# Optimization experiments

Hardware: AMD Instinct MI355X
Metric: run time of the kernel (lower is better)

Reference implementation:

```python
import jax, jax.numpy as jnp
import numpy as np

B, POMO, PROB, EMB, H, D = 64, 200, 200, 512, 16, 32
SQRT_EMB = 22.627416997969522  # sqrt(512)
CLIP = 10.0


def _heads(x):
    # (b, n, H*D) -> (b, H, n, D)
    b, n, _ = x.shape
    return x.reshape(b, n, H, D).transpose(0, 2, 1, 3)


def setup_inputs() -> dict:
    key = jax.random.key(0)
    ks = jax.random.split(key, 10)
    s = 1.0 / np.sqrt(EMB)
    return {
        "encoded_nodes": jax.random.normal(ks[0], (B, PROB + 1, EMB), jnp.float32),
        "encoded_q1": jax.random.normal(ks[1], (B, POMO, EMB), jnp.float32),
        "encoded_last_node": jax.random.normal(ks[2], (B, POMO, EMB), jnp.float32),
        "ninf_mask": jnp.zeros((B, POMO, PROB), jnp.float32),
        "Wq_first": jax.random.normal(ks[3], (EMB, H * D), jnp.float32) * s,
        "Wq_last": jax.random.normal(ks[4], (EMB, H * D), jnp.float32) * s,
        "Wk": jax.random.normal(ks[5], (EMB, H * D), jnp.float32) * s,
        "Wv": jax.random.normal(ks[6], (EMB, H * D), jnp.float32) * s,
        "Wc": jax.random.normal(ks[7], (H * D, EMB), jnp.float32) * s,
        "bc": jax.random.normal(ks[8], (EMB,), jnp.float32) * 0.01,
    }


def reference(encoded_nodes, encoded_q1, encoded_last_node, ninf_mask,
              Wq_first, Wq_last, Wk, Wv, Wc, bc):
    # set_kv
    k = _heads(encoded_nodes @ Wk)            # (b, H, prob+1, D)
    v = _heads(encoded_nodes @ Wv)            # (b, H, prob+1, D)
    single_head_key = encoded_nodes[:, :-1]   # (b, prob, emb)
    # set_q1 + forward queries
    q = _heads(encoded_q1 @ Wq_first) + _heads(encoded_last_node @ Wq_last)  # (b, H, pomo, D)
    # masked multi-head attention; mask padded with a zero column for the depot/last node
    mask3 = jnp.concatenate([ninf_mask, jnp.zeros((B, POMO, 1), ninf_mask.dtype)], axis=-1)
    score = jnp.einsum('bhnd,bhmd->bhnm', q, k) / jnp.sqrt(jnp.float32(D))
    weights = jax.nn.softmax(score + mask3[:, None, :, :], axis=-1)
    out = jnp.einsum('bhnm,bhmd->bhnd', weights, v)        # (b, H, pomo, D)
    out_concat = out.transpose(0, 2, 1, 3).reshape(B, POMO, H * D)
    mh_atten_out = out_concat @ Wc + bc                    # (b, pomo, emb)
    # single-head pointer score with tanh clipping
    score2 = jnp.einsum('bne,bpe->bnp', mh_atten_out, single_head_key) / SQRT_EMB
    score_masked = CLIP * jnp.tanh(score2) + ninf_mask
    return jax.nn.softmax(score_masked, axis=2)            # (b, pomo, prob)
```

## Files before the change

kernel.cpp:

```cpp
#include <hip/hip_runtime.h>
#include <cstdint>
#include <cstddef>

typedef _Float16 f16;
typedef f16 f16x4 __attribute__((ext_vector_type(4)));
typedef f16 f16x8 __attribute__((ext_vector_type(8)));
typedef float f32x4 __attribute__((ext_vector_type(4)));

#define NB    64
#define NPOMO 200
#define NNODE 201
#define NEMB  512
#define NH    16
#define ND    32
#define VTSTR 208

__device__ __forceinline__ void gload16(const void* g, void* l) {
  __builtin_amdgcn_global_load_lds((const __attribute__((address_space(1))) void*)g,
                                   (__attribute__((address_space(3))) void*)l, 16, 0, 0);
}


__global__ void prep_kernel(const float* __restrict__ enc, const float* __restrict__ q1,
                            const float* __restrict__ ql, const float* __restrict__ Wk,
                            const float* __restrict__ Wv, const float* __restrict__ Wqf,
                            const float* __restrict__ Wql, const float* __restrict__ Wc,
                            f16* __restrict__ Xnh, f16* __restrict__ Qcat,
                            f16* __restrict__ wkvT, f16* __restrict__ wqT,
                            f16* __restrict__ wcT) {
  const int bx = blockIdx.x;
  const int tid = threadIdx.x;
  if (bx < 6432) {
    int i = bx * 256 + tid;
    if (i < 1646592) {
      float4 v = ((const float4*)enc)[i];
      f16x4 h = {(f16)v.x, (f16)v.y, (f16)v.z, (f16)v.w};
      ((f16x4*)Xnh)[i] = h;
    }
  } else if (bx < 19232) {
    int i = (bx - 6432) * 256 + tid;
    int row = i >> 8;
    int g = i & 255;
    const float* src = (g < 128) ? (q1 + (size_t)row * 512 + g * 4)
                                 : (ql + (size_t)row * 512 + (g - 128) * 4);
    float4 v = *(const float4*)src;
    f16x4 h = {(f16)v.x, (f16)v.y, (f16)v.z, (f16)v.w};
    ((f16x4*)Qcat)[i] = h;
  } else {
    int i = (bx - 19232) * 256 + tid;
    if (i < 524288) {
      int j = i >> 9, k = i & 511;
      float v = (j < 512) ? Wk[(size_t)k * 512 + j] : Wv[(size_t)k * 512 + (j - 512)];
      wkvT[i] = (f16)v;
    } else if (i < 1048576) {
      int t = i - 524288;
      int j = t >> 10, k = t & 1023;
      float v = (k < 512) ? Wqf[(size_t)k * 512 + j] : Wql[(size_t)(k - 512) * 512 + j];
      wqT[t] = (f16)v;
    } else if (i < 1310720) {
      int t = i - 1048576;
      int j = t >> 9, k = t & 511;
      wcT[t] = (f16)Wc[(size_t)k * 512 + j];
    }
  }
}


__device__ __forceinline__ void gemm_body512(
    const f16* __restrict__ A, const f16* __restrict__ B, f16* __restrict__ C,
    int M, int K, int m0, int n0, f16* As, f16* Bs, f16* __restrict__ vtp) {
  const int tid = threadIdx.x;
  const int wave = tid >> 6, lane = tid & 63;
  const int qd = lane >> 4, c = lane & 15;
  const int wm = wave >> 2, wn = wave & 3;

  f32x4 acc[4][4];
#pragma unroll
  for (int i = 0; i < 4; ++i)
#pragma unroll
    for (int j = 0; j < 4; ++j) acc[i][j] = (f32x4){0.f, 0.f, 0.f, 0.f};

  for (int kc = 0; kc < K; kc += 64) {
#pragma unroll
    for (int i = 0; i < 2; ++i) {
      int id = tid + i * 512;
      int row = id >> 3, sj = id & 7;
      int gr = m0 + row; if (gr >= M) gr = M - 1;
      int gj = sj ^ (row & 7);
      gload16(A + (size_t)gr * K + kc + gj * 8, As + id * 8);
    }
#pragma unroll
    for (int i = 0; i < 4; ++i) {
      int id = tid + i * 512;
      int row = id >> 3, sj = id & 7;
      int gj = sj ^ (row & 7);
      gload16(B + (size_t)(n0 + row) * K + kc + gj * 8, Bs + id * 8);
    }
    __syncthreads();
#pragma unroll
    for (int kk = 0; kk < 2; ++kk) {
      f16x8 af[4], bf[4];
#pragma unroll
      for (int t = 0; t < 4; ++t) {
        int ra = wm * 64 + t * 16 + c;
        af[t] = *(const f16x8*)(As + ra * 64 + (((kk * 4 + qd) ^ (ra & 7)) * 8));
        int rb = wn * 64 + t * 16 + c;
        bf[t] = *(const f16x8*)(Bs + rb * 64 + (((kk * 4 + qd) ^ (rb & 7)) * 8));
      }
#pragma unroll
      for (int mt = 0; mt < 4; ++mt)
#pragma unroll
        for (int nt = 0; nt < 4; ++nt)
          acc[mt][nt] = __builtin_amdgcn_mfma_f32_16x16x32_f16(af[mt], bf[nt], acc[mt][nt], 0, 0, 0);
    }
    __syncthreads();
  }

#pragma unroll
  for (int mt = 0; mt < 4; ++mt) {
#pragma unroll
    for (int nt = 0; nt < 4; ++nt) {
      int col = n0 + wn * 64 + nt * 16 + c;
#pragma unroll
      for (int r = 0; r < 4; ++r) {
        int row = m0 + wm * 64 + mt * 16 + qd * 4 + r;
        if (row < M) {
          f16 hv = (f16)acc[mt][nt][r];
          if (!vtp) {
            C[(size_t)row * 512 + col] = hv;
          } else if (col < 512) {
            C[(size_t)row * 512 + col] = hv;
          } else {
            int bb = row / 201, node = row - bb * 201;
            int hd = col - 512;
            vtp[(((size_t)(bb * NH) + (hd >> 5)) * 32 + (hd & 31)) * VTSTR + node] = hv;
          }
        }
      }
    }
  }
}

__global__ __launch_bounds__(512, 4) void gemm_proj(
    const f16* __restrict__ Xnh, const f16* __restrict__ WkvT, f16* __restrict__ Kp,
    f16* __restrict__ VT, const f16* __restrict__ Qcat, const f16* __restrict__ WqT,
    f16* __restrict__ Qp) {
  __shared__ f16 As[128 * 64];
  __shared__ f16 Bs[256 * 64];
  const int bx = blockIdx.x;
  if (bx < 200) {
    gemm_body512(Qcat, WqT, Qp, 12800, 1024, (bx % 100) * 128, (bx / 100) * 256, As, Bs, nullptr);
  } else {
    int t = bx - 200;
    gemm_body512(Xnh, WkvT, Kp, 12864, 512, (t % 101) * 128, (t / 101) * 256, As, Bs, VT);
  }
}


__device__ __forceinline__ void gemm_body(
    const f16* __restrict__ A, const f16* __restrict__ B, f16* __restrict__ C,
    const float* __restrict__ bias, int M, int N, int K, int m0, int n0,
    f16* As, f16* Bs) {
  const int tid = threadIdx.x;
  const int wave = tid >> 6, lane = tid & 63;
  const int qd = lane >> 4, c = lane & 15;
  const int wm = wave >> 1, wn = wave & 1;
  const int srow = lane >> 3, sj = lane & 7;

  f32x4 acc[4][4];
#pragma unroll
  for (int i = 0; i < 4; ++i)
#pragma unroll
    for (int j = 0; j < 4; ++j) acc[i][j] = (f32x4){0.f, 0.f, 0.f, 0.f};

  for (int kc = 0; kc < K; kc += 64) {
#pragma unroll
    for (int i = 0; i < 4; ++i) {
      int row = wave * 32 + i * 8 + srow;
      int gr = m0 + row; if (gr >= M) gr = M - 1;
      int gj = sj ^ (row & 7);
      gload16(A + (size_t)gr * K + kc + gj * 8, As + row * 64 + sj * 8);
    }
#pragma unroll
    for (int i = 0; i < 4; ++i) {
      int row = wave * 32 + i * 8 + srow;
      int gj = sj ^ (row & 7);
      gload16(B + (size_t)(n0 + row) * K + kc + gj * 8, Bs + row * 64 + sj * 8);
    }
    __syncthreads();
#pragma unroll
    for (int kk = 0; kk < 2; ++kk) {
      f16x8 af[4], bf[4];
#pragma unroll
      for (int t = 0; t < 4; ++t) {
        int ra = wm * 64 + t * 16 + c;
        af[t] = *(const f16x8*)(As + ra * 64 + (((kk * 4 + qd) ^ (ra & 7)) * 8));
        int rb = wn * 64 + t * 16 + c;
        bf[t] = *(const f16x8*)(Bs + rb * 64 + (((kk * 4 + qd) ^ (rb & 7)) * 8));
      }
#pragma unroll
      for (int mt = 0; mt < 4; ++mt)
#pragma unroll
        for (int nt = 0; nt < 4; ++nt)
          acc[mt][nt] = __builtin_amdgcn_mfma_f32_16x16x32_f16(af[mt], bf[nt], acc[mt][nt], 0, 0, 0);
    }
    __syncthreads();
  }

#pragma unroll
  for (int mt = 0; mt < 4; ++mt) {
#pragma unroll
    for (int nt = 0; nt < 4; ++nt) {
      int col = n0 + wn * 64 + nt * 16 + c;
      float bv = bias ? bias[col] : 0.0f;
#pragma unroll
      for (int r = 0; r < 4; ++r) {
        int row = m0 + wm * 64 + mt * 16 + qd * 4 + r;
        if (row < M) C[(size_t)row * N + col] = (f16)(acc[mt][nt][r] + bv);
      }
    }
  }
}

__global__ __launch_bounds__(256, 2) void gemm_wc(
    const f16* __restrict__ Oc, const f16* __restrict__ WcT, f16* __restrict__ mhb,
    const float* __restrict__ bc) {
  __shared__ f16 As[128 * 64];
  __shared__ f16 Bs[128 * 64];
  const int bx = blockIdx.x;
  gemm_body(Oc, WcT, mhb, bc, 12800, 512, 512, (bx % 100) * 128, (bx / 100) * 128, As, Bs);
}


__global__ __launch_bounds__(256, 4) void attn_kernel(
    const f16* __restrict__ Qp, const f16* __restrict__ Kp,
    const f16* __restrict__ VT, const float* __restrict__ mask,
    f16* __restrict__ Oc) {
  const int bid = blockIdx.x;
  const int hg = bid & 3;
  const int rt = (bid >> 2) % 13;
  const int b = bid / 52;
  const int wave = threadIdx.x >> 6, lane = threadIdx.x & 63;
  const int qd = lane >> 4, c = lane & 15;
  const int h = hg * 4 + wave;

  const int r0 = rt * 16;
  const int qrow = min(r0 + c, 199);
  const float scale = 0.17677669529663687f;

  f16x8 aq = *(const f16x8*)(Qp + ((size_t)(b * NPOMO + qrow)) * 512 + h * 32 + qd * 8);

  f32x4 s[13];
#pragma unroll
  for (int nt = 0; nt < 13; ++nt) {
    int node = nt * 16 + c; if (node > 200) node = 200;
    f16x8 ak = *(const f16x8*)(Kp + ((size_t)(b * NNODE + node)) * 512 + h * 32 + qd * 8);
    f32x4 z = (f32x4){0.f, 0.f, 0.f, 0.f};
    s[nt] = __builtin_amdgcn_mfma_f32_16x16x32_f16(ak, aq, z, 0, 0, 0);
  }

  float mx = -3e38f;
#pragma unroll
  for (int nt = 0; nt < 13; ++nt) {
    const int col0 = nt * 16 + qd * 4;
    float4 mv = make_float4(0.f, 0.f, 0.f, 0.f);
    if (col0 < 200)
      mv = *(const float4*)(mask + ((size_t)b * NPOMO + qrow) * 200 + col0);
#pragma unroll
    for (int r = 0; r < 4; ++r) {
      int node = col0 + r;
      float v;
      if (node > 200)      v = -3e38f;
      else if (node == 200) v = s[nt][r] * scale;
      else                  v = s[nt][r] * scale + ((const float*)&mv)[r];
      s[nt][r] = v;
      mx = fmaxf(mx, v);
    }
  }
  mx = fmaxf(mx, __shfl_xor(mx, 16));
  mx = fmaxf(mx, __shfl_xor(mx, 32));

  float sm = 0.f;
  f16x4 pf[13];
#pragma unroll
  for (int nt = 0; nt < 13; ++nt) {
    f16x4 p4;
#pragma unroll
    for (int r = 0; r < 4; ++r) {
      float p = __expf(s[nt][r] - mx);
      sm += p;
      p4[r] = (f16)p;
    }
    pf[nt] = p4;
  }
  sm += __shfl_xor(sm, 16);
  sm += __shfl_xor(sm, 32);
  const float inv = 1.0f / sm;

  const f16* vbase = VT + ((size_t)(b * NH + h)) * 32 * VTSTR;
  f32x4 o0 = (f32x4){0.f, 0.f, 0.f, 0.f};
  f32x4 o1 = (f32x4){0.f, 0.f, 0.f, 0.f};
#pragma unroll
  for (int nt = 0; nt < 13; ++nt) {
    const int nb = nt * 16 + qd * 4;
    f16x4 av0 = *(const f16x4*)(vbase + c * VTSTR + nb);
    f16x4 av1 = *(const f16x4*)(vbase + (c + 16) * VTSTR + nb);
    o0 = __builtin_amdgcn_mfma_f32_16x16x16f16(av0, pf[nt], o0, 0, 0, 0);
    o1 = __builtin_amdgcn_mfma_f32_16x16x16f16(av1, pf[nt], o1, 0, 0, 0);
  }

  const int row = r0 + c;
  if (row < 200) {
    f16* dst = Oc + ((size_t)(b * NPOMO + row)) * 512 + h * 32 + qd * 4;
    f16x4 w0 = {(f16)(o0[0] * inv), (f16)(o0[1] * inv), (f16)(o0[2] * inv), (f16)(o0[3] * inv)};
    f16x4 w1 = {(f16)(o1[0] * inv), (f16)(o1[1] * inv), (f16)(o1[2] * inv), (f16)(o1[3] * inv)};
    *(f16x4*)dst = w0;
    *(f16x4*)(dst + 16) = w1;
  }
}


__global__ __launch_bounds__(256, 4) void final_kernel(
    const f16* __restrict__ mh, const f16* __restrict__ Xnh,
    const float* __restrict__ mask, float* __restrict__ out) {
  __shared__ float xmax[4][16];
  __shared__ float xsum[4][16];
  const int b = blockIdx.x / 13;
  const int tile = blockIdx.x % 13;
  const int r0 = tile * 16;
  const int tid = threadIdx.x;
  const int wave = tid >> 6, lane = tid & 63;
  const int qd = lane >> 4, c = lane & 15;

  const int nt0 = (wave == 0) ? 0 : (3 * wave + 1);
  const int cnt = (wave == 0) ? 4 : 3;

  const int qrow = min(r0 + c, 199);
  const size_t rbase = ((size_t)(b * NPOMO + qrow)) * 512;

  size_t abase[4];
#pragma unroll
  for (int i = 0; i < 4; ++i) {
    int nt = nt0 + i;
    int nd = nt * 16 + c; if (nd > 200) nd = 200;
    abase[i] = ((size_t)(b * NNODE + nd)) * 512;
  }

  f32x4 acc[4];
#pragma unroll
  for (int i = 0; i < 4; ++i) acc[i] = (f32x4){0.f, 0.f, 0.f, 0.f};

#pragma unroll 4
  for (int kc = 0; kc < 512; kc += 32) {
    f16x8 bq = *(const f16x8*)(mh + rbase + kc + qd * 8);
#pragma unroll
    for (int i = 0; i < 4; ++i) {
      if (i < cnt) {
        f16x8 a = *(const f16x8*)(Xnh + abase[i] + kc + qd * 8);
        acc[i] = __builtin_amdgcn_mfma_f32_16x16x32_f16(a, bq, acc[i], 0, 0, 0);
      }
    }
  }

  const float invS = 1.0f / 22.627416997969522f;
  float mx = -3e38f;
#pragma unroll
  for (int i = 0; i < 4; ++i) {
    if (i >= cnt) break;
    const int nt = nt0 + i;
    const int col0 = nt * 16 + qd * 4;
    float4 mv = make_float4(0.f, 0.f, 0.f, 0.f);
    if (col0 < 200)
      mv = *(const float4*)(mask + ((size_t)b * NPOMO + qrow) * 200 + col0);
#pragma unroll
    for (int r = 0; r < 4; ++r) {
      int node = col0 + r;
      float v;
      if (node < 200) {
        float t = __expf(2.0f * acc[i][r] * invS);
        float th = 1.0f - 2.0f / (t + 1.0f);
        v = 10.0f * th + ((const float*)&mv)[r];
      } else {
        v = -3e38f;
      }
      acc[i][r] = v;
      mx = fmaxf(mx, v);
    }
  }
  mx = fmaxf(mx, __shfl_xor(mx, 16));
  mx = fmaxf(mx, __shfl_xor(mx, 32));
  if (lane < 16) xmax[wave][lane] = mx;
  __syncthreads();
  mx = fmaxf(fmaxf(xmax[0][c], xmax[1][c]), fmaxf(xmax[2][c], xmax[3][c]));

  float sm = 0.f;
#pragma unroll
  for (int i = 0; i < 4; ++i) {
    if (i >= cnt) break;
#pragma unroll
    for (int r = 0; r < 4; ++r) {
      float p = __expf(acc[i][r] - mx);
      acc[i][r] = p;
      sm += p;
    }
  }
  sm += __shfl_xor(sm, 16);
  sm += __shfl_xor(sm, 32);
  if (lane < 16) xsum[wave][lane] = sm;
  __syncthreads();
  const float tot = xsum[0][c] + xsum[1][c] + xsum[2][c] + xsum[3][c];
  const float inv = 1.0f / tot;

  const int row = r0 + c;
  if (row < 200) {
#pragma unroll
    for (int i = 0; i < 4; ++i) {
      if (i >= cnt) break;
      const int col0 = (nt0 + i) * 16 + qd * 4;
      if (col0 < 200) {
        float4 o;
        o.x = acc[i][0] * inv; o.y = acc[i][1] * inv;
        o.z = acc[i][2] * inv; o.w = acc[i][3] * inv;
        *(float4*)(out + ((size_t)b * NPOMO + row) * 200 + col0) = o;
      }
    }
  }
}


extern "C" void kernel_launch(void* const* d_in, const int* in_sizes, int n_in,
                              void* d_out, int out_size, void* d_ws, size_t ws_size,
                              hipStream_t stream) {
  (void)in_sizes; (void)n_in; (void)out_size; (void)ws_size;
  const float* enc   = (const float*)d_in[0];
  const float* q1    = (const float*)d_in[1];
  const float* qlast = (const float*)d_in[2];
  const float* mask  = (const float*)d_in[3];
  const float* Wqf   = (const float*)d_in[4];
  const float* Wql   = (const float*)d_in[5];
  const float* Wk    = (const float*)d_in[6];
  const float* Wv    = (const float*)d_in[7];
  const float* Wc    = (const float*)d_in[8];
  const float* bc    = (const float*)d_in[9];
  float* out = (float*)d_out;

  char* ws = (char*)d_ws;
  f16* Xnh  = (f16*)(ws + 0);
  f16* Qcat = (f16*)(ws + 13172736);
  f16* WkvT = (f16*)(ws + 39387136);
  f16* WqT  = (f16*)(ws + 40435712);
  f16* WcT  = (f16*)(ws + 41484288);
  f16* Kp   = (f16*)(ws + 42008576);
  f16* VT   = (f16*)(ws + 55181312);
  f16* Qp   = (f16*)(ws + 68812800);
  f16* Oc   = (f16*)(ws + 81920000);
  f16* mhb  = (f16*)(ws + 95027200);

  hipLaunchKernelGGL(prep_kernel, dim3(24352), dim3(256), 0, stream,
                     enc, q1, qlast, Wk, Wv, Wqf, Wql, Wc, Xnh, Qcat, WkvT, WqT, WcT);
  hipLaunchKernelGGL(gemm_proj, dim3(604), dim3(512), 0, stream,
                     Xnh, WkvT, Kp, VT, Qcat, WqT, Qp);
  hipLaunchKernelGGL(attn_kernel, dim3(3328), dim3(256), 0, stream, Qp, Kp, VT, mask, Oc);
  hipLaunchKernelGGL(gemm_wc, dim3(400), dim3(256), 0, stream, Oc, WcT, mhb, bc);
  hipLaunchKernelGGL(final_kernel, dim3(832), dim3(256), 0, stream, mhb, Xnh, mask, out);
}
```

Measured before the change: 297.5 us.

## Load GEMM A operand directly from global into registers and swizzle block order

Drops the shared-memory staging of the A operand in both projection GEMMs and the Wc GEMM. Each wave now reads its A fragments straight from global memory into registers, and only B goes through LDS. Block indices are remapped into groups of 8 M-tiles that share N tiles, to improve L2 reuse. Freeing the LDS lets gemm_wc raise its occupancy hint from 2 to 4 blocks. The risk is more global-load latency exposed in the inner loop, with uncoalesced 16-byte row reads.

```diff
diff --git a/kernel.cpp b/kernel.cpp
--- a/kernel.cpp
+++ b/kernel.cpp
@@ -68,12 +68,19 @@
 
 __device__ __forceinline__ void gemm_body512(
     const f16* __restrict__ A, const f16* __restrict__ B, f16* __restrict__ C,
-    int M, int K, int m0, int n0, f16* As, f16* Bs, f16* __restrict__ vtp) {
+    int M, int K, int m0, int n0, f16* Bs, f16* __restrict__ vtp) {
   const int tid = threadIdx.x;
   const int wave = tid >> 6, lane = tid & 63;
   const int qd = lane >> 4, c = lane & 15;
   const int wm = wave >> 2, wn = wave & 3;
 
+  const f16* arow[4];
+#pragma unroll
+  for (int t = 0; t < 4; ++t) {
+    int gr = m0 + wm * 64 + t * 16 + c; if (gr >= M) gr = M - 1;
+    arow[t] = A + (size_t)gr * K;
+  }
+
   f32x4 acc[4][4];
 #pragma unroll
   for (int i = 0; i < 4; ++i)
@@ -81,14 +88,6 @@
     for (int j = 0; j < 4; ++j) acc[i][j] = (f32x4){0.f, 0.f, 0.f, 0.f};
 
   for (int kc = 0; kc < K; kc += 64) {
-#pragma unroll
-    for (int i = 0; i < 2; ++i) {
-      int id = tid + i * 512;
-      int row = id >> 3, sj = id & 7;
-      int gr = m0 + row; if (gr >= M) gr = M - 1;
-      int gj = sj ^ (row & 7);
-      gload16(A + (size_t)gr * K + kc + gj * 8, As + id * 8);
-    }
 #pragma unroll
     for (int i = 0; i < 4; ++i) {
       int id = tid + i * 512;
@@ -101,9 +100,10 @@
     for (int kk = 0; kk < 2; ++kk) {
       f16x8 af[4], bf[4];
 #pragma unroll
+      for (int t = 0; t < 4; ++t)
+        af[t] = *(const f16x8*)(arow[t] + kc + kk * 32 + qd * 8);
+#pragma unroll
       for (int t = 0; t < 4; ++t) {
-        int ra = wm * 64 + t * 16 + c;
-        af[t] = *(const f16x8*)(As + ra * 64 + (((kk * 4 + qd) ^ (ra & 7)) * 8));
         int rb = wn * 64 + t * 16 + c;
         bf[t] = *(const f16x8*)(Bs + rb * 64 + (((kk * 4 + qd) ^ (rb & 7)) * 8));
       }
@@ -145,27 +145,43 @@
     const f16* __restrict__ Xnh, const f16* __restrict__ WkvT, f16* __restrict__ Kp,
     f16* __restrict__ VT, const f16* __restrict__ Qcat, const f16* __restrict__ WqT,
     f16* __restrict__ Qp) {
-  __shared__ f16 As[128 * 64];
   __shared__ f16 Bs[256 * 64];
   const int bx = blockIdx.x;
   if (bx < 200) {
-    gemm_body512(Qcat, WqT, Qp, 12800, 1024, (bx % 100) * 128, (bx / 100) * 256, As, Bs, nullptr);
+    int m, n;
+    if (bx < 192) { m = (bx >> 4) * 8 + (bx & 7); n = (bx >> 3) & 1; }
+    else { int t = bx - 192; m = 96 + (t >> 1); n = t & 1; }
+    gemm_body512(Qcat, WqT, Qp, 12800, 1024, m * 128, n * 256, Bs, nullptr);
   } else {
-    int t = bx - 200;
-    gemm_body512(Xnh, WkvT, Kp, 12864, 512, (t % 101) * 128, (t / 101) * 256, As, Bs, VT);
-  }
-}
-
-
-__device__ __forceinline__ void gemm_body(
-    const f16* __restrict__ A, const f16* __restrict__ B, f16* __restrict__ C,
-    const float* __restrict__ bias, int M, int N, int K, int m0, int n0,
-    f16* As, f16* Bs) {
+    int t = bx - 200, m, n;
+    if (t < 384) { m = (t >> 5) * 8 + (t & 7); n = (t >> 3) & 3; }
+    else { int tt = t - 384; m = 96 + (tt >> 2); n = tt & 3; }
+    gemm_body512(Xnh, WkvT, Kp, 12864, 512, m * 128, n * 256, Bs, VT);
+  }
+}
+
+
+__global__ __launch_bounds__(256, 4) void gemm_wc(
+    const f16* __restrict__ Oc, const f16* __restrict__ WcT, f16* __restrict__ mhb,
+    const float* __restrict__ bc) {
+  __shared__ f16 Bs[128 * 64];
+  const int bx = blockIdx.x;
+  int m, n;
+  if (bx < 384) { m = (bx >> 5) * 8 + (bx & 7); n = (bx >> 3) & 3; }
+  else { int tt = bx - 384; m = 96 + (tt >> 2); n = tt & 3; }
+  const int m0 = m * 128, n0 = n * 128;
+
   const int tid = threadIdx.x;
   const int wave = tid >> 6, lane = tid & 63;
   const int qd = lane >> 4, c = lane & 15;
   const int wm = wave >> 1, wn = wave & 1;
-  const int srow = lane >> 3, sj = lane & 7;
+
+  const f16* arow[4];
+#pragma unroll
+  for (int t = 0; t < 4; ++t) {
+    int gr = m0 + wm * 64 + t * 16 + c; if (gr >= 12800) gr = 12799;
+    arow[t] = Oc + (size_t)gr * 512;
+  }
 
   f32x4 acc[4][4];
 #pragma unroll
@@ -173,28 +189,23 @@
 #pragma unroll
     for (int j = 0; j < 4; ++j) acc[i][j] = (f32x4){0.f, 0.f, 0.f, 0.f};
 
-  for (int kc = 0; kc < K; kc += 64) {
+  for (int kc = 0; kc < 512; kc += 64) {
 #pragma unroll
     for (int i = 0; i < 4; ++i) {
-      int row = wave * 32 + i * 8 + srow;
-      int gr = m0 + row; if (gr >= M) gr = M - 1;
+      int id = tid + i * 256;
+      int row = id >> 3, sj = id & 7;
       int gj = sj ^ (row & 7);
-      gload16(A + (size_t)gr * K + kc + gj * 8, As + row * 64 + sj * 8);
-    }
-#pragma unroll
-    for (int i = 0; i < 4; ++i) {
-      int row = wave * 32 + i * 8 + srow;
-      int gj = sj ^ (row & 7);
-      gload16(B + (size_t)(n0 + row) * K + kc + gj * 8, Bs + row * 64 + sj * 8);
+      gload16(WcT + (size_t)(n0 + row) * 512 + kc + gj * 8, Bs + id * 8);
     }
     __syncthreads();
 #pragma unroll
     for (int kk = 0; kk < 2; ++kk) {
       f16x8 af[4], bf[4];
 #pragma unroll
+      for (int t = 0; t < 4; ++t)
+        af[t] = *(const f16x8*)(arow[t] + kc + kk * 32 + qd * 8);
+#pragma unroll
       for (int t = 0; t < 4; ++t) {
-        int ra = wm * 64 + t * 16 + c;
-        af[t] = *(const f16x8*)(As + ra * 64 + (((kk * 4 + qd) ^ (ra & 7)) * 8));
         int rb = wn * 64 + t * 16 + c;
         bf[t] = *(const f16x8*)(Bs + rb * 64 + (((kk * 4 + qd) ^ (rb & 7)) * 8));
       }
@@ -212,23 +223,14 @@
 #pragma unroll
     for (int nt = 0; nt < 4; ++nt) {
       int col = n0 + wn * 64 + nt * 16 + c;
-      float bv = bias ? bias[col] : 0.0f;
+      float bv = bc[col];
 #pragma unroll
       for (int r = 0; r < 4; ++r) {
         int row = m0 + wm * 64 + mt * 16 + qd * 4 + r;
-        if (row < M) C[(size_t)row * N + col] = (f16)(acc[mt][nt][r] + bv);
-      }
-    }
-  }
-}
-
-__global__ __launch_bounds__(256, 2) void gemm_wc(
-    const f16* __restrict__ Oc, const f16* __restrict__ WcT, f16* __restrict__ mhb,
-    const float* __restrict__ bc) {
-  __shared__ f16 As[128 * 64];
-  __shared__ f16 Bs[128 * 64];
-  const int bx = blockIdx.x;
-  gemm_body(Oc, WcT, mhb, bc, 12800, 512, 512, (bx % 100) * 128, (bx / 100) * 128, As, Bs);
+        if (row < 12800) mhb[(size_t)row * 512 + col] = (f16)(acc[mt][nt][r] + bv);
+      }
+    }
+  }
 }
 
 
```

Measured after the change: 351.0 us. 18.0% more time.
